# Kernel optimization log

Measured on AMD Instinct MI355X. Metric: run time of the kernel, lower is better.

## Reference

```python
import jax, jax.numpy as jnp
import numpy as np

EMBED_DIM = 1024
NUM_HEADS = 16
HEAD_DIM = EMBED_DIM // NUM_HEADS
SCALE = HEAD_DIM ** (-0.5)
CLAMP = 50000.0
MASK_FILL = -9e15


def setup_inputs() -> dict:
    key = jax.random.key(0)
    ks = jax.random.split(key, 12)
    B, Lq, Lk = 4, 1024, 1024
    q = jax.random.normal(ks[0], (B, Lq, EMBED_DIM), dtype=jnp.float32)
    k = jax.random.normal(ks[1], (B, Lk, EMBED_DIM), dtype=jnp.float32)
    v = jax.random.normal(ks[2], (B, Lk, EMBED_DIM), dtype=jnp.float32)
    attention_mask = jax.random.randint(ks[3], (B, Lk), 0, 2, dtype=jnp.int32)
    s = 0.02  # xavier-ish scale
    Wq = jax.random.normal(ks[4], (EMBED_DIM, EMBED_DIM), dtype=jnp.float32) * s
    Wk = jax.random.normal(ks[5], (EMBED_DIM, EMBED_DIM), dtype=jnp.float32) * s
    Wv = jax.random.normal(ks[6], (EMBED_DIM, EMBED_DIM), dtype=jnp.float32) * s
    Wo = jax.random.normal(ks[7], (EMBED_DIM, EMBED_DIM), dtype=jnp.float32) * s
    bq = jnp.zeros((EMBED_DIM,), jnp.float32)
    bk = jnp.zeros((EMBED_DIM,), jnp.float32)
    bv = jnp.zeros((EMBED_DIM,), jnp.float32)
    bo = jnp.zeros((EMBED_DIM,), jnp.float32)
    return {"q": q, "k": k, "v": v, "attention_mask": attention_mask,
            "Wq": Wq, "bq": bq, "Wk": Wk, "bk": bk,
            "Wv": Wv, "bv": bv, "Wo": Wo, "bo": bo}


def _split_heads(x, B, L):
    # [B, L, E] -> [B, H, L, D]
    return x.reshape(B, L, NUM_HEADS, HEAD_DIM).transpose(0, 2, 1, 3)


def reference(q, k, v, attention_mask, Wq, bq, Wk, bk, Wv, bv, Wo, bo):
    B, Lq, _ = q.shape
    Lk = k.shape[1]
    # projections (Linear: x @ W.T + b), query pre-scaled as in source
    qs = _split_heads((q @ Wq.T + bq) * SCALE, B, Lq)   # [B,H,Lq,D]
    ks = _split_heads(k @ Wk.T + bk, B, Lk)             # [B,H,Lk,D]
    vs = _split_heads(v @ Wv.T + bv, B, Lk)             # [B,H,Lk,D]
    logits = jnp.einsum('bhqd,bhkd->bhqk', qs, ks)      # [B,H,Lq,Lk]
    logits = jnp.clip(logits, -CLAMP, CLAMP)
    # mask: where 0 -> large negative, else the mask value itself is added
    m = attention_mask.astype(logits.dtype)
    madd = jnp.where(attention_mask == 0, MASK_FILL, m)[:, None, None, :]
    logits = logits + madd
    attn = jax.nn.softmax(logits, axis=-1)              # [B,H,Lq,Lk]
    out = jnp.einsum('bhqk,bhkd->bhqd', attn, vs)       # dropout is eval-mode identity
    out = out.transpose(0, 2, 1, 3).reshape(B, Lq, EMBED_DIM)
    out = out @ Wo.T + bo
    return out, attn
```

## Files before the change

kernel.cpp:

```cpp
#include <hip/hip_runtime.h>

typedef __attribute__((ext_vector_type(8))) short s16x8;
typedef __attribute__((ext_vector_type(4))) short s16x4;
typedef __attribute__((ext_vector_type(4))) float f32x4;

#define DEVI __device__ __forceinline__

DEVI unsigned short f2bf(float f){
  unsigned int u = __float_as_uint(f);
  return (unsigned short)((u + 0x7fffu + ((u >> 16) & 1u)) >> 16);
}

DEVI s16x8 mk8(s16x4 a, s16x4 b){
  s16x8 r;
  r[0]=a[0]; r[1]=a[1]; r[2]=a[2]; r[3]=a[3];
  r[4]=b[0]; r[5]=b[1]; r[6]=b[2]; r[7]=b[3];
  return r;
}

DEVI f32x4 mfma16(s16x8 a, s16x8 b, f32x4 c){
  return __builtin_amdgcn_mfma_f32_16x16x32_bf16(a, b, c, 0, 0, 0);
}

DEVI void gload16(const unsigned short* g, unsigned short* l){
  __builtin_amdgcn_global_load_lds((const __attribute__((address_space(1))) void*)g,
                                   (__attribute__((address_space(3))) void*)l, 16, 0, 0);
}

__global__ __launch_bounds__(256) void cvt_all_k(
    const float* __restrict__ q, const float* __restrict__ k, const float* __restrict__ v,
    const float* __restrict__ wq, const float* __restrict__ wk,
    const float* __restrict__ wv, const float* __restrict__ wo,
    unsigned short* __restrict__ ws)
{
  int bi = blockIdx.x, tid = threadIdx.x;
  const float* src; unsigned short* dst; int base;
  if (bi < 3072){
    int t = bi >> 10;
    src = (t==0) ? q : ((t==1) ? k : v);
    dst = ws + t*4194304;
    base = (bi & 1023) * 4096;
  } else {
    int t = (bi - 3072) >> 8;
    src = (t==0) ? wq : ((t==1) ? wk : ((t==2) ? wv : wo));
    dst = ws + 12582912 + t*1048576;
    base = ((bi - 3072) & 255) * 4096;
  }
  #pragma unroll
  for (int it = 0; it < 4; ++it){
    int i = base + it*1024 + tid*4;
    float4 f = *(const float4*)(src + i);
    s16x4 o;
    o[0] = (short)f2bf(f.x); o[1] = (short)f2bf(f.y);
    o[2] = (short)f2bf(f.z); o[3] = (short)f2bf(f.w);
    *(s16x4*)(dst + i) = o;
  }
}

__global__ __launch_bounds__(256) void proj_k(
    const unsigned short* __restrict__ Xall, const unsigned short* __restrict__ Wall,
    const float* __restrict__ bq, const float* __restrict__ bk, const float* __restrict__ bv,
    unsigned short* __restrict__ QK, unsigned short* __restrict__ Vt)
{
  __shared__ unsigned short Asm[2][4096];
  __shared__ unsigned short Bsm[2][4096];
  const int tid = threadIdx.x, lane = tid & 63;
  const int w = tid >> 6, g = lane >> 4, ln = lane & 15;
  const int z = blockIdx.z;
  const int m0 = blockIdx.y * 128, n0 = blockIdx.x * 128;
  const int wm = w >> 1, wn = w & 1;
  const unsigned short* A  = Xall + z * 4194304;
  const unsigned short* Bw = Wall + z * 1048576;
  const float* bias = (z==0) ? bq : ((z==1) ? bk : bv);

  f32x4 acc[4][4];
  #pragma unroll
  for (int i=0;i<4;++i)
    #pragma unroll
    for (int j=0;j<4;++j) acc[i][j] = (f32x4){0.f,0.f,0.f,0.f};

  auto stage = [&](int buf, int kt){
    #pragma unroll
    for (int r=0;r<2;++r){
      int c = r*256 + tid;
      int row = c >> 2, cs = (c & 3) ^ ((row >> 1) & 3);
      gload16(A + (m0+row)*1024 + kt*32 + cs*8, &Asm[buf][(r*256 + (tid & 192))*8]);
    }
    #pragma unroll
    for (int r=0;r<2;++r){
      int c = r*256 + tid;
      int row = c >> 2, cs = (c & 3) ^ ((row >> 1) & 3);
      gload16(Bw + (n0+row)*1024 + kt*32 + cs*8, &Bsm[buf][(r*256 + (tid & 192))*8]);
    }
  };

  stage(0, 0);
  for (int kt = 0; kt < 32; ++kt){
    __syncthreads();
    if (kt + 1 < 32) stage((kt+1)&1, kt+1);
    const unsigned short* As = Asm[kt&1];
    const unsigned short* Bs = Bsm[kt&1];
    s16x8 af[4], bfr[4];
    #pragma unroll
    for (int mf=0; mf<4; ++mf){
      int row = wm*64 + mf*16 + ln;
      af[mf] = *(const s16x8*)(As + row*32 + ((g ^ ((row>>1)&3))<<3));
    }
    #pragma unroll
    for (int nf=0; nf<4; ++nf){
      int row = wn*64 + nf*16 + ln;
      bfr[nf] = *(const s16x8*)(Bs + row*32 + ((g ^ ((row>>1)&3))<<3));
    }
    if (z < 2){
      #pragma unroll
      for (int i=0; i<4; ++i)
        #pragma unroll
        for (int j=0; j<4; ++j)
          acc[i][j] = mfma16(bfr[i], af[j], acc[i][j]);
    } else {
      #pragma unroll
      for (int i=0; i<4; ++i)
        #pragma unroll
        for (int j=0; j<4; ++j)
          acc[i][j] = mfma16(af[i], bfr[j], acc[i][j]);
    }
  }

  if (z < 2){
    unsigned short* O = QK + z * 4194304;
    #pragma unroll
    for (int i=0; i<4; ++i){
      int fb = n0 + wn*64 + i*16 + g*4;
      f32x4 b4 = *(const f32x4*)&bias[fb];
      int hh = fb >> 6, d = fb & 63;
      #pragma unroll
      for (int j=0; j<4; ++j){
        int token = m0 + wm*64 + j*16 + ln;
        int bb = token >> 10, l = token & 1023;
        s16x4 o;
        #pragma unroll
        for (int r=0;r<4;++r){
          float val = acc[i][j][r] + b4[r];
          if (z == 0) val *= 0.125f;
          o[r] = (short)f2bf(val);
        }
        *(s16x4*)(&O[((bb*16 + hh)*1024 + l)*64 + d]) = o;
      }
    }
  } else {
    #pragma unroll
    for (int nf=0; nf<4; ++nf){
      int n = n0 + wn*64 + nf*16 + ln;
      float bv_ = bias[n];
      int hh = n >> 6, d = n & 63;
      #pragma unroll
      for (int mf=0; mf<4; ++mf){
        int mb = m0 + wm*64 + mf*16 + g*4;
        int bb = mb >> 10, l = mb & 1023;
        s16x4 o;
        #pragma unroll
        for (int r=0;r<4;++r) o[r] = (short)f2bf(acc[mf][nf][r] + bv_);
        *(s16x4*)(Vt + ((bb*16 + hh)*64 + d)*1024 + l) = o;
      }
    }
  }
}

__global__ __launch_bounds__(256) void attn_k(
    const unsigned short* __restrict__ Qp, const unsigned short* __restrict__ Kp,
    const unsigned short* __restrict__ Vt, const int* __restrict__ mask,
    float* __restrict__ attn, unsigned short* __restrict__ Ob)
{
  __shared__ unsigned short Qs[4096];
  __shared__ unsigned short Ks[2][4096];
  __shared__ unsigned short Vs[2][4096];
  __shared__ float madd[1024];

  const int tid = threadIdx.x, lane = tid & 63;
  const int w = tid >> 6, g = lane >> 4, ln = lane & 15;
  const int qt = blockIdx.x, bh = blockIdx.y, b = bh >> 4, h = bh & 15;
  const int q0 = qt * 64;

  auto stage64 = [&](unsigned short* dstbuf, const unsigned short* srcbase, int rowStride){
    #pragma unroll
    for (int r=0;r<2;++r){
      int c = r*256 + tid;
      int row = c >> 3, cs = (c & 7) ^ (row & 7);
      gload16(srcbase + row*rowStride + cs*8, dstbuf + (r*256 + (tid & 192))*8);
    }
  };

  stage64(Qs, Qp + (bh*1024 + q0)*64, 64);
  stage64(Ks[0], Kp + bh*65536, 64);
  {
    int4 mv = *(const int4*)(mask + b*1024 + tid*4);
    f32x4 md;
    md[0] = mv.x ? (float)mv.x : -9e15f;
    md[1] = mv.y ? (float)mv.y : -9e15f;
    md[2] = mv.z ? (float)mv.z : -9e15f;
    md[3] = mv.w ? (float)mv.w : -9e15f;
    *(f32x4*)(&madd[tid*4]) = md;
  }
  __syncthreads();

  s16x8 qf[2];
  {
    int row = w*16 + ln;
    #pragma unroll
    for (int ks=0; ks<2; ++ks)
      qf[ks] = *(const s16x8*)(Qs + row*64 + (((ks*4 + g) ^ (row & 7)) << 3));
  }

  float rsum = 0.f;
  for (int kt = 0; kt < 16; ++kt){
    if (kt + 1 < 16) stage64(Ks[(kt+1)&1], Kp + bh*65536 + (kt+1)*4096, 64);
    const unsigned short* Kc = Ks[kt&1];
    f32x4 sacc[4];
    #pragma unroll
    for (int nf=0;nf<4;++nf) sacc[nf] = (f32x4){0.f,0.f,0.f,0.f};
    __builtin_amdgcn_s_setprio(1);
    #pragma unroll
    for (int ks=0; ks<2; ++ks){
      #pragma unroll
      for (int nf=0; nf<4; ++nf){
        int row = nf*16 + ln;
        s16x8 kf = *(const s16x8*)(Kc + row*64 + (((ks*4 + g) ^ (row & 7)) << 3));
        sacc[nf] = mfma16(kf, qf[ks], sacc[nf]);
      }
    }
    __builtin_amdgcn_s_setprio(0);
    #pragma unroll
    for (int nf=0; nf<4; ++nf){
      f32x4 md = *(const f32x4*)&madd[kt*64 + nf*16 + g*4];
      #pragma unroll
      for (int r=0;r<4;++r){
        float s = fminf(fmaxf(sacc[nf][r], -50000.f), 50000.f);
        rsum += __expf(s + md[r]);
      }
    }
    __syncthreads();
  }
  rsum += __shfl_xor(rsum, 16);
  rsum += __shfl_xor(rsum, 32);
  const float inv = (rsum > 0.f) ? (1.f / rsum) : 0.f;

  stage64(Ks[0], Kp + bh*65536, 64);
  stage64(Vs[0], Vt + bh*65536, 1024);
  __syncthreads();

  f32x4 oacc[4];
  #pragma unroll
  for (int dt=0;dt<4;++dt) oacc[dt] = (f32x4){0.f,0.f,0.f,0.f};

  float* arow = attn + (bh*1024 + q0 + w*16 + ln)*1024;

  for (int kt = 0; kt < 16; ++kt){
    if (kt + 1 < 16){
      stage64(Ks[(kt+1)&1], Kp + bh*65536 + (kt+1)*4096, 64);
      stage64(Vs[(kt+1)&1], Vt + bh*65536 + (kt+1)*64, 1024);
    }
    const unsigned short* Kc = Ks[kt&1];
    const unsigned short* Vc = Vs[kt&1];
    f32x4 sacc[4];
    #pragma unroll
    for (int nf=0;nf<4;++nf) sacc[nf] = (f32x4){0.f,0.f,0.f,0.f};
    __builtin_amdgcn_s_setprio(1);
    #pragma unroll
    for (int ks=0; ks<2; ++ks){
      #pragma unroll
      for (int nf=0; nf<4; ++nf){
        int row = nf*16 + ln;
        s16x8 kf = *(const s16x8*)(Kc + row*64 + (((ks*4 + g) ^ (row & 7)) << 3));
        sacc[nf] = mfma16(kf, qf[ks], sacc[nf]);
      }
    }
    __builtin_amdgcn_s_setprio(0);
    s16x4 pb[4];
    #pragma unroll
    for (int nf=0; nf<4; ++nf){
      f32x4 md = *(const f32x4*)&madd[kt*64 + nf*16 + g*4];
      f32x4 av;
      #pragma unroll
      for (int r=0;r<4;++r){
        float s = fminf(fmaxf(sacc[nf][r], -50000.f), 50000.f);
        float p = __expf(s + md[r]);
        pb[nf][r] = (short)f2bf(p);
        av[r] = p * inv;
      }
      *(f32x4*)(arow + kt*64 + nf*16 + g*4) = av;
    }
    s16x8 pf0 = mk8(pb[0], pb[1]);
    s16x8 pf1 = mk8(pb[2], pb[3]);
    __builtin_amdgcn_s_setprio(1);
    #pragma unroll
    for (int ks=0; ks<2; ++ks){
      s16x8 pfc = ks ? pf1 : pf0;
      #pragma unroll
      for (int dt=0; dt<4; ++dt){
        int row = dt*16 + ln, xr = (row & 7) << 1;
        const unsigned short* vp = Vc + row*64;
        s16x4 lo = *(const s16x4*)(vp + (((ks*8 + g) ^ xr) << 2));
        s16x4 hi = *(const s16x4*)(vp + (((ks*8 + g + 4) ^ xr) << 2));
        oacc[dt] = mfma16(mk8(lo, hi), pfc, oacc[dt]);
      }
    }
    __builtin_amdgcn_s_setprio(0);
    __syncthreads();
  }

  #pragma unroll
  for (int dt=0; dt<4; ++dt){
    s16x4 o;
    #pragma unroll
    for (int r=0;r<4;++r) o[r] = (short)f2bf(oacc[dt][r] * inv);
    *(s16x4*)(Ob + (b*1024 + q0 + w*16 + ln)*1024 + h*64 + dt*16 + g*4) = o;
  }
}

__global__ __launch_bounds__(256) void outproj_k(
    const unsigned short* __restrict__ A, const unsigned short* __restrict__ Bw,
    const float* __restrict__ bias, float* __restrict__ O)
{
  __shared__ unsigned short Asm[2][4096];
  __shared__ unsigned short Bsm[2][4096];
  const int tid = threadIdx.x, lane = tid & 63;
  const int w = tid >> 6, g = lane >> 4, ln = lane & 15;
  const int m0 = blockIdx.y * 128, n0 = blockIdx.x * 128;
  const int wm = w >> 1, wn = w & 1;

  f32x4 acc[4][4];
  #pragma unroll
  for (int i=0;i<4;++i)
    #pragma unroll
    for (int j=0;j<4;++j) acc[i][j] = (f32x4){0.f,0.f,0.f,0.f};

  auto stage = [&](int buf, int kt){
    #pragma unroll
    for (int r=0;r<2;++r){
      int c = r*256 + tid;
      int row = c >> 2, cs = (c & 3) ^ ((row >> 1) & 3);
      gload16(A + (m0+row)*1024 + kt*32 + cs*8, &Asm[buf][(r*256 + (tid & 192))*8]);
    }
    #pragma unroll
    for (int r=0;r<2;++r){
      int c = r*256 + tid;
      int row = c >> 2, cs = (c & 3) ^ ((row >> 1) & 3);
      gload16(Bw + (n0+row)*1024 + kt*32 + cs*8, &Bsm[buf][(r*256 + (tid & 192))*8]);
    }
  };

  stage(0, 0);
  for (int kt = 0; kt < 32; ++kt){
    __syncthreads();
    if (kt + 1 < 32) stage((kt+1)&1, kt+1);
    const unsigned short* As = Asm[kt&1];
    const unsigned short* Bs = Bsm[kt&1];
    s16x8 af[4], bfr[4];
    #pragma unroll
    for (int mf=0; mf<4; ++mf){
      int row = wm*64 + mf*16 + ln;
      af[mf] = *(const s16x8*)(As + row*32 + ((g ^ ((row>>1)&3))<<3));
    }
    #pragma unroll
    for (int nf=0; nf<4; ++nf){
      int row = wn*64 + nf*16 + ln;
      bfr[nf] = *(const s16x8*)(Bs + row*32 + ((g ^ ((row>>1)&3))<<3));
    }
    #pragma unroll
    for (int i=0; i<4; ++i)
      #pragma unroll
      for (int j=0; j<4; ++j)
        acc[i][j] = mfma16(bfr[i], af[j], acc[i][j]);
  }

  #pragma unroll
  for (int i=0; i<4; ++i){
    int fb = n0 + wn*64 + i*16 + g*4;
    f32x4 b4 = *(const f32x4*)&bias[fb];
    #pragma unroll
    for (int j=0; j<4; ++j){
      int token = m0 + wm*64 + j*16 + ln;
      f32x4 ov;
      #pragma unroll
      for (int r=0;r<4;++r) ov[r] = acc[i][j][r] + b4[r];
      *(f32x4*)(&O[token*1024 + fb]) = ov;
    }
  }
}

extern "C" void kernel_launch(void* const* d_in, const int* in_sizes, int n_in,
                              void* d_out, int out_size, void* d_ws, size_t ws_size,
                              hipStream_t stream) {
  (void)in_sizes; (void)n_in; (void)out_size; (void)ws_size;
  const float* q  = (const float*)d_in[0];
  const float* k  = (const float*)d_in[1];
  const float* v  = (const float*)d_in[2];
  const int* mask = (const int*)d_in[3];
  const float* Wq = (const float*)d_in[4];  const float* bq = (const float*)d_in[5];
  const float* Wk = (const float*)d_in[6];  const float* bk = (const float*)d_in[7];
  const float* Wv = (const float*)d_in[8];  const float* bv = (const float*)d_in[9];
  const float* Wo = (const float*)d_in[10]; const float* bo = (const float*)d_in[11];

  unsigned short* ws = (unsigned short*)d_ws;
  unsigned short* xb   = ws;
  unsigned short* wb   = ws + 12582912;
  unsigned short* Qp   = ws + 16777216;
  unsigned short* Vtb  = ws + 25165824;
  unsigned short* Ob   = ws;

  float* outp  = (float*)d_out;
  float* attnp = outp + 4194304;

  cvt_all_k<<<4096, 256, 0, stream>>>(q, k, v, Wq, Wk, Wv, Wo, ws);
  proj_k<<<dim3(8, 32, 3), 256, 0, stream>>>(xb, wb, bq, bk, bv, Qp, Vtb);
  attn_k<<<dim3(16, 64), 256, 0, stream>>>(Qp, Qp + 4194304, Vtb, mask, attnp, Ob);
  outproj_k<<<dim3(8, 32), 256, 0, stream>>>(Ob, wb + 3145728, bo, outp);
}
```

Before: 497.4 us.

## Load Q/K/V fragments directly from global memory instead of LDS staging

The attention kernel drops its LDS double-buffered staging of Q, K and V tiles and has each lane read its MFMA fragments straight from global memory, relying on L1/L2 caching across the four waves that share the same K/V tiles. This removes the per-tile __syncthreads barriers and frees most of the shared memory, and a launch-bounds occupancy hint of 4 blocks is added. In exchange every wave issues redundant global loads with no prefetch, so load latency is exposed directly in the MFMA loop and cache bandwidth pressure rises.

```diff
diff --git a/kernel.cpp b/kernel.cpp
--- a/kernel.cpp
+++ b/kernel.cpp
@@ -166,14 +166,11 @@
   }
 }
 
-__global__ __launch_bounds__(256) void attn_k(
+__global__ __launch_bounds__(256, 4) void attn_k(
     const unsigned short* __restrict__ Qp, const unsigned short* __restrict__ Kp,
     const unsigned short* __restrict__ Vt, const int* __restrict__ mask,
     float* __restrict__ attn, unsigned short* __restrict__ Ob)
 {
-  __shared__ unsigned short Qs[4096];
-  __shared__ unsigned short Ks[2][4096];
-  __shared__ unsigned short Vs[2][4096];
   __shared__ float madd[1024];
 
   const int tid = threadIdx.x, lane = tid & 63;
@@ -181,17 +178,9 @@
   const int qt = blockIdx.x, bh = blockIdx.y, b = bh >> 4, h = bh & 15;
   const int q0 = qt * 64;
 
-  auto stage64 = [&](unsigned short* dstbuf, const unsigned short* srcbase, int rowStride){
-    #pragma unroll
-    for (int r=0;r<2;++r){
-      int c = r*256 + tid;
-      int row = c >> 3, cs = (c & 7) ^ (row & 7);
-      gload16(srcbase + row*rowStride + cs*8, dstbuf + (r*256 + (tid & 192))*8);
-    }
-  };
-
-  stage64(Qs, Qp + (bh*1024 + q0)*64, 64);
-  stage64(Ks[0], Kp + bh*65536, 64);
+  const unsigned short* Kg = Kp + bh*65536;
+  const unsigned short* Vg = Vt + bh*65536;
+
   {
     int4 mv = *(const int4*)(mask + b*1024 + tid*4);
     f32x4 md;
@@ -201,20 +190,18 @@
     md[3] = mv.w ? (float)mv.w : -9e15f;
     *(f32x4*)(&madd[tid*4]) = md;
   }
-  __syncthreads();
 
   s16x8 qf[2];
   {
-    int row = w*16 + ln;
+    int qrow = q0 + w*16 + ln;
     #pragma unroll
     for (int ks=0; ks<2; ++ks)
-      qf[ks] = *(const s16x8*)(Qs + row*64 + (((ks*4 + g) ^ (row & 7)) << 3));
-  }
+      qf[ks] = *(const s16x8*)(Qp + (bh*1024 + qrow)*64 + (ks*4 + g)*8);
+  }
+  __syncthreads();
 
   float rsum = 0.f;
   for (int kt = 0; kt < 16; ++kt){
-    if (kt + 1 < 16) stage64(Ks[(kt+1)&1], Kp + bh*65536 + (kt+1)*4096, 64);
-    const unsigned short* Kc = Ks[kt&1];
     f32x4 sacc[4];
     #pragma unroll
     for (int nf=0;nf<4;++nf) sacc[nf] = (f32x4){0.f,0.f,0.f,0.f};
@@ -223,8 +210,7 @@
     for (int ks=0; ks<2; ++ks){
       #pragma unroll
       for (int nf=0; nf<4; ++nf){
-        int row = nf*16 + ln;
-        s16x8 kf = *(const s16x8*)(Kc + row*64 + (((ks*4 + g) ^ (row & 7)) << 3));
+        s16x8 kf = *(const s16x8*)(Kg + (kt*64 + nf*16 + ln)*64 + (ks*4 + g)*8);
         sacc[nf] = mfma16(kf, qf[ks], sacc[nf]);
       }
     }
@@ -238,16 +224,11 @@
         rsum += __expf(s + md[r]);
       }
     }
-    __syncthreads();
   }
   rsum += __shfl_xor(rsum, 16);
   rsum += __shfl_xor(rsum, 32);
   const float inv = (rsum > 0.f) ? (1.f / rsum) : 0.f;
 
-  stage64(Ks[0], Kp + bh*65536, 64);
-  stage64(Vs[0], Vt + bh*65536, 1024);
-  __syncthreads();
-
   f32x4 oacc[4];
   #pragma unroll
   for (int dt=0;dt<4;++dt) oacc[dt] = (f32x4){0.f,0.f,0.f,0.f};
@@ -255,12 +236,6 @@
   float* arow = attn + (bh*1024 + q0 + w*16 + ln)*1024;
 
   for (int kt = 0; kt < 16; ++kt){
-    if (kt + 1 < 16){
-      stage64(Ks[(kt+1)&1], Kp + bh*65536 + (kt+1)*4096, 64);
-      stage64(Vs[(kt+1)&1], Vt + bh*65536 + (kt+1)*64, 1024);
-    }
-    const unsigned short* Kc = Ks[kt&1];
-    const unsigned short* Vc = Vs[kt&1];
     f32x4 sacc[4];
     #pragma unroll
     for (int nf=0;nf<4;++nf) sacc[nf] = (f32x4){0.f,0.f,0.f,0.f};
@@ -269,8 +244,7 @@
     for (int ks=0; ks<2; ++ks){
       #pragma unroll
       for (int nf=0; nf<4; ++nf){
-        int row = nf*16 + ln;
-        s16x8 kf = *(const s16x8*)(Kc + row*64 + (((ks*4 + g) ^ (row & 7)) << 3));
+        s16x8 kf = *(const s16x8*)(Kg + (kt*64 + nf*16 + ln)*64 + (ks*4 + g)*8);
         sacc[nf] = mfma16(kf, qf[ks], sacc[nf]);
       }
     }
@@ -297,15 +271,13 @@
       s16x8 pfc = ks ? pf1 : pf0;
       #pragma unroll
       for (int dt=0; dt<4; ++dt){
-        int row = dt*16 + ln, xr = (row & 7) << 1;
-        const unsigned short* vp = Vc + row*64;
-        s16x4 lo = *(const s16x4*)(vp + (((ks*8 + g) ^ xr) << 2));
-        s16x4 hi = *(const s16x4*)(vp + (((ks*8 + g + 4) ^ xr) << 2));
+        const unsigned short* vp = Vg + (dt*16 + ln)*1024 + kt*64 + ks*32 + g*4;
+        s16x4 lo = *(const s16x4*)(vp);
+        s16x4 hi = *(const s16x4*)(vp + 16);
         oacc[dt] = mfma16(mk8(lo, hi), pfc, oacc[dt]);
       }
     }
     __builtin_amdgcn_s_setprio(0);
-    __syncthreads();
   }
 
   #pragma unroll
```

After: 645.4 us. 1.3x slower.
